# Kernel tuning notes

Hardware: AMD Instinct MI355X
Metric: run time of the kernel (lower is better)

## Reference

```python
import jax, jax.numpy as jnp
import numpy as np

D_MODEL = 512
NUM_HEADS = 8
D_K = D_MODEL // NUM_HEADS
D_FF = 2048
VOCAB = 32000
PAD_IDX = 0
SEQ = 2048
BATCH = 8
N_REPEAT = 6
# source computes ((d_model/num_heads)**1)/2 = 32.0 (precedence bug), not sqrt(d_k)
SCORE_DIV = (D_MODEL / NUM_HEADS) / 2.0
LN_EPS = 1e-5


def setup_inputs() -> dict:
    key = jax.random.key(0)
    ks = jax.random.split(key, 16)
    s = lambda fan_in: 1.0 / np.sqrt(fan_in)
    inp = {
        "ids": jax.random.randint(ks[0], (BATCH, SEQ), 0, VOCAB, dtype=jnp.int64)
               if jax.config.jax_enable_x64 else
               jax.random.randint(ks[0], (BATCH, SEQ), 0, VOCAB, dtype=jnp.int32),
        "emb": jax.random.normal(ks[1], (VOCAB, D_MODEL), jnp.float32),
        "Wq": jax.random.normal(ks[2], (D_MODEL, D_K), jnp.float32) * s(D_MODEL),
        "bq": jnp.zeros((D_K,), jnp.float32),
        "Wk": jax.random.normal(ks[3], (D_MODEL, D_K), jnp.float32) * s(D_MODEL),
        "bk": jnp.zeros((D_K,), jnp.float32),
        "Wv": jax.random.normal(ks[4], (D_MODEL, D_K), jnp.float32) * s(D_MODEL),
        "bv": jnp.zeros((D_K,), jnp.float32),
        "Wo": jax.random.normal(ks[5], (D_MODEL, D_MODEL), jnp.float32) * s(D_MODEL),
        "bo": jnp.zeros((D_MODEL,), jnp.float32),
        "W1": jax.random.normal(ks[6], (D_MODEL, D_FF), jnp.float32) * s(D_MODEL),
        "b1": jnp.zeros((D_FF,), jnp.float32),
        "W2": jax.random.normal(ks[7], (D_FF, D_MODEL), jnp.float32) * s(D_FF),
        "b2": jnp.zeros((D_MODEL,), jnp.float32),
    }
    # padding_idx row is zero in torch's nn.Embedding
    inp["emb"] = inp["emb"].at[PAD_IDX].set(0.0)
    return inp


def positional_encoding(seq_len, d_model):
    pos = jnp.arange(seq_len, dtype=jnp.float32)[:, None]          # [S,1]
    even_i = jnp.arange(0, d_model, 2, dtype=jnp.float32)          # actual indices 0,2,4,...
    odd_i = jnp.arange(1, d_model, 2, dtype=jnp.float32)
    pe_even = jnp.sin(pos / jnp.power(10000.0, 2.0 * even_i / d_model))  # [S,D/2]
    pe_odd = jnp.cos(pos / jnp.power(10000.0, 2.0 * odd_i / d_model))    # [S,D/2]
    pe = jnp.stack([pe_even, pe_odd], axis=2).reshape(seq_len, d_model)  # interleave
    return pe[None]  # [1,S,D]


def whole_tensor_layernorm(x):
    # F.layer_norm(x, normalized_shape=x.shape): normalize over ALL elems, no affine
    m = jnp.mean(x)
    v = jnp.mean(jnp.square(x - m))
    return (x - m) * jax.lax.rsqrt(v + LN_EPS)


def encoder_forward(ids, emb, Wq, bq, Wk, bk, Wv, bv, Wo, bo, W1, b1, W2, b2):
    mask = (ids != PAD_IDX)[..., None].astype(emb.dtype)
    x = emb[ids] * mask + positional_encoding(ids.shape[1], D_MODEL)  # [B,S,D]
    for _ in range(N_REPEAT):  # same weights reused every repeat (as in source)
        # all heads use the SAME q/k/v Linear -> compute once, tile NUM_HEADS times
        q = jnp.einsum("bsd,dk->bsk", x, Wq) + bq   # [B,S,64]
        k = jnp.einsum("bsd,dk->bsk", x, Wk) + bk
        v = jnp.einsum("bsd,dk->bsk", x, Wv) + bv
        scores = jnp.einsum("bsk,btk->bst", q, k) / SCORE_DIV  # [B,S,S]
        attn = jax.nn.softmax(scores, axis=-1)
        head = jnp.einsum("bst,btk->bsk", attn, v)             # [B,S,64]
        concat = jnp.tile(head, (1, 1, NUM_HEADS))             # [B,S,512]
        mha = jnp.einsum("bsd,de->bse", concat, Wo) + bo
        x1 = whole_tensor_layernorm(mha + x)
        ff = jnp.einsum("bsd,df->bsf", jax.nn.relu(jnp.einsum("bsd,df->bsf", x1, W1) + b1), W2) + b2
        x = whole_tensor_layernorm(x1 + ff)
    return x


def reference(ids, emb, Wq, bq, Wk, bk, Wv, bv, Wo, bo, W1, b1, W2, b2):
    return encoder_forward(ids, emb, Wq, bq, Wk, bk, Wv, bv, Wo, bo, W1, b1, W2, b2)
```

## Files before the change

kernel.cpp:

```cpp
#include <hip/hip_runtime.h>
#include <math.h>

#define BB 8
#define SS 2048
#define DM 512
#define DK 64
#define DFF 2048
#define ROWS (BB*SS)
#define NTOT (ROWS*DM)
#define LN_EPS 1e-5
#define PAD_IDX 0

typedef __attribute__((ext_vector_type(8))) short short8;
typedef __attribute__((ext_vector_type(4))) short s16x4;
typedef __attribute__((ext_vector_type(4))) float f32x4;

__device__ __forceinline__ short f2b(float f) {
    unsigned u = __float_as_uint(f);
    unsigned r = (u + 0x7fffu + ((u >> 16) & 1u)) >> 16;
    return (short)r;
}
__device__ __forceinline__ float b2f(short s) {
    return __uint_as_float(((unsigned)(unsigned short)s) << 16);
}

__global__ __launch_bounds__(256) void embed_kernel(const int* __restrict__ ids,
                                                    const float* __restrict__ emb,
                                                    short* __restrict__ T1,
                                                    double* __restrict__ red) {
    int idx = blockIdx.x * 256 + threadIdx.x;
    if (idx < 24) red[idx] = 0.0;
    if (idx >= NTOT) return;
    int d   = idx & (DM - 1);
    int row = idx >> 9;
    int s   = row & (SS - 1);
    int id  = ids[row];
    float e = (id != PAD_IDX) ? emb[(size_t)id * DM + d] : 0.0f;
    float ex  = 2.0f * (float)d / 512.0f;
    float div = powf(10000.0f, ex);
    float arg = (float)s / div;
    float pe  = (d & 1) ? cosf(arg) : sinf(arg);
    T1[idx] = f2b(e + pe);
}

__global__ __launch_bounds__(256) void packqkvT_kernel(const float* __restrict__ Wq,
                                                       const float* __restrict__ Wk,
                                                       const float* __restrict__ Wv,
                                                       const float* __restrict__ bq,
                                                       const float* __restrict__ bk,
                                                       const float* __restrict__ bv,
                                                       short* __restrict__ WqkvT,
                                                       float* __restrict__ bqkv) {
    int i = blockIdx.x * 256 + threadIdx.x;
    if (i < 256 * 512) {
        int n = i >> 9, k = i & 511;
        float v = (n < 64)  ? Wq[k * 64 + n]
                : (n < 128) ? Wk[k * 64 + (n - 64)]
                : (n < 192) ? Wv[k * 64 + (n - 128)] : 0.0f;
        WqkvT[i] = f2b(v);
    }
    if (i < 256)
        bqkv[i] = (i < 64) ? bq[i] : (i < 128) ? bk[i - 64] : (i < 192) ? bv[i - 128] : 0.0f;
}

__global__ __launch_bounds__(256) void wosumT_kernel(const float* __restrict__ Wo,
                                                     short* __restrict__ WoST) {
    int i = blockIdx.x * 256 + threadIdx.x;
    if (i >= 512 * 64) return;
    int e = i >> 6, k = i & 63;
    float s = 0.f;
#pragma unroll
    for (int h = 0; h < 8; ++h) s += Wo[(size_t)(h * 64 + k) * 512 + e];
    WoST[i] = f2b(s);
}

__global__ __launch_bounds__(256) void transpose_b16(const float* __restrict__ in,
                                                     short* __restrict__ out,
                                                     int R, int C) {
    __shared__ float tile[32][33];
    int bx = blockIdx.x * 32;
    int by = blockIdx.y * 32;
    int tx = threadIdx.x & 31, ty = threadIdx.x >> 5;
#pragma unroll
    for (int i = 0; i < 32; i += 8)
        tile[ty + i][tx] = in[(size_t)(by + ty + i) * C + bx + tx];
    __syncthreads();
#pragma unroll
    for (int i = 0; i < 32; i += 8)
        out[(size_t)(bx + ty + i) * R + by + tx] = f2b(tile[tx][ty + i]);
}

__global__ __launch_bounds__(256) void colsum_kernel(const short* __restrict__ WqkvT,
                                                     const short* __restrict__ W1T,
                                                     float* __restrict__ csq,
                                                     float* __restrict__ csw1) {
    int i = blockIdx.x * 256 + threadIdx.x;
    if (i < 256) {
        const short* p = WqkvT + (size_t)i * 512;
        float s = 0.f;
        for (int k = 0; k < 512; ++k) s += b2f(p[k]);
        csq[i] = s;
    } else if (i < 2304) {
        int n = i - 256;
        const short* p = W1T + (size_t)n * 512;
        float s = 0.f;
        for (int k = 0; k < 512; ++k) s += b2f(p[k]);
        csw1[n] = s;
    }
}

__global__ __launch_bounds__(256) void vtrans_kernel(const short* __restrict__ qkvb,
                                                     short* __restrict__ Vtg) {
    __shared__ short tile[32][40];
    int sx = blockIdx.x * 32;
    int dy = blockIdx.y * 32;
    int b  = blockIdx.z;
    int tx = threadIdx.x & 31, ty = threadIdx.x >> 5;
#pragma unroll
    for (int i = 0; i < 32; i += 8)
        tile[ty + i][tx] = qkvb[(size_t)(b * SS + sx + ty + i) * 256 + 128 + dy + tx];
    __syncthreads();
#pragma unroll
    for (int i = 0; i < 32; i += 8)
        Vtg[(size_t)(b * 64 + dy + ty + i) * SS + sx + tx] = tile[tx][ty + i];
}

__device__ __forceinline__ void async16(const void* g, void* l) {
    __builtin_amdgcn_global_load_lds(
        (const __attribute__((address_space(1))) void*)g,
        (__attribute__((address_space(3))) void*)l, 16, 0, 0);
}

template <bool RELU, bool RESID, bool STATS, bool FOLD, int BM, int BN, int BK>
__global__ __launch_bounds__(256) void gemm_mfma(const short* __restrict__ A,
                                                 const short* __restrict__ BT,
                                                 const float* __restrict__ bias,
                                                 const float* __restrict__ colsum,
                                                 const short* __restrict__ residB,
                                                 short* __restrict__ C,
                                                 const double* __restrict__ statsIn,
                                                 double* __restrict__ statsOut,
                                                 int M, int N, int K) {
    constexpr int NT   = (BN == 256) ? 4 : ((BM == 128) ? 4 : 2);
    constexpr int KSUB = BK / 32;
    constexpr int RPS  = (BK == 32) ? 64 : 32;
    constexpr int LPS  = (BM + BN) / RPS;
    __shared__ short As[2][BM * BK];
    __shared__ short Bs[2][BN * BK];
    const int t   = threadIdx.x;
    const int wv  = t >> 6;
    const int l   = t & 63;
    const int q   = l >> 4,  l16 = l & 15;
    const int mbase = (BM == 128) ? (wv >> 1) * 64 : 0;
    const int nbase = (BM == 128) ? (wv & 1) * 64
                    : ((BN == 256) ? wv * 64 : wv * 32);
    const long m0 = (long)blockIdx.x * BM;
    const long n0 = (long)blockIdx.y * BN;

    float muf = 0.f, rstdf = 1.f;
    if (FOLD || RESID) {
        if (statsIn) {
            double mean = statsIn[0] * (1.0 / NTOT);
            double var  = statsIn[1] * (1.0 / NTOT) - mean * mean;
            muf   = (float)mean;
            rstdf = (float)(1.0 / sqrt(var + LN_EPS));
        }
    }

    f32x4 acc[4][NT] = {};

    const int srow = (BK == 32) ? (wv * 16 + (l >> 2)) : (wv * 8 + (l >> 3));
    const int kcol = (BK == 32) ? (((l & 3) ^ ((l >> 3) & 3)) * 8)
                                : (((l & 7) ^ ((l >> 3) & 7)) * 8);
    const int wrow = (BK == 32) ? wv * 16 : wv * 8;

    auto stage = [&](int buf, int k0) {
#pragma unroll
        for (int i = 0; i < BM / RPS; ++i)
            async16(A + (m0 + srow + i * RPS) * (long)K + k0 + kcol,
                    &As[buf][(wrow + i * RPS) * BK + l * 8]);
#pragma unroll
        for (int i = 0; i < BN / RPS; ++i)
            async16(BT + (n0 + srow + i * RPS) * (long)K + k0 + kcol,
                    &Bs[buf][(wrow + i * RPS) * BK + l * 8]);
    };

    stage(0, 0);
    if (K > BK) stage(1, BK);
    int cur = 0;
    for (int k0 = 0; k0 < K; k0 += BK) {
        if (k0 + BK < K) {
            if constexpr (LPS == 3)       asm volatile("s_waitcnt vmcnt(3)" ::: "memory");
            else if constexpr (LPS == 4)  asm volatile("s_waitcnt vmcnt(4)" ::: "memory");
            else if constexpr (LPS == 6)  asm volatile("s_waitcnt vmcnt(6)" ::: "memory");
            else if constexpr (LPS == 8)  asm volatile("s_waitcnt vmcnt(8)" ::: "memory");
            else                          asm volatile("s_waitcnt vmcnt(10)" ::: "memory");
        } else {
            asm volatile("s_waitcnt vmcnt(0)" ::: "memory");
        }
        __builtin_amdgcn_sched_barrier(0);
        __builtin_amdgcn_s_barrier();
        __builtin_amdgcn_sched_barrier(0);

        short8 af[KSUB][4], bfr[KSUB][NT];
#pragma unroll
        for (int ks = 0; ks < KSUB; ++ks) {
            const int slot = (BK == 32) ? (q ^ ((l16 >> 1) & 3))
                                        : ((ks * 4 + q) ^ (l16 & 7));
#pragma unroll
            for (int i = 0; i < 4; ++i)
                af[ks][i] = *(const short8*)&As[cur][(mbase + i * 16 + l16) * BK + slot * 8];
#pragma unroll
            for (int i = 0; i < NT; ++i)
                bfr[ks][i] = *(const short8*)&Bs[cur][(nbase + i * 16 + l16) * BK + slot * 8];
        }
        asm volatile("s_waitcnt lgkmcnt(0)" ::: "memory");
        __builtin_amdgcn_sched_barrier(0);
        __builtin_amdgcn_s_barrier();
        __builtin_amdgcn_sched_barrier(0);

        if (k0 + 2 * BK < K) stage(cur, k0 + 2 * BK);

        __builtin_amdgcn_s_setprio(1);
#pragma unroll
        for (int ks = 0; ks < KSUB; ++ks)
#pragma unroll
            for (int mt = 0; mt < 4; ++mt)
#pragma unroll
                for (int nt = 0; nt < NT; ++nt)
                    acc[mt][nt] = __builtin_amdgcn_mfma_f32_16x16x32_bf16(
                        af[ks][mt], bfr[ks][nt], acc[mt][nt], 0, 0, 0);
        __builtin_amdgcn_s_setprio(0);
        cur ^= 1;
    }

    const float mr = muf * rstdf;
    float s = 0.f, sq = 0.f;
#pragma unroll
    for (int mt = 0; mt < 4; ++mt) {
        const long rowb = m0 + mbase + mt * 16 + q * 4;
#pragma unroll
        for (int nt = 0; nt < NT; ++nt) {
            const long col = n0 + nbase + nt * 16 + l16;
            const float bv = bias[col];
            const float cs = FOLD ? colsum[col] : 0.f;
#pragma unroll
            for (int r = 0; r < 4; ++r) {
                const long idx = (rowb + r) * (long)N + col;
                float v = acc[mt][nt][r];
                if (FOLD) v = rstdf * v + bv - mr * cs;
                else      v = v + bv;
                if (RESID) v += (b2f(residB[idx]) - muf) * rstdf;
                if (RELU)  v = fmaxf(v, 0.0f);
                if (STATS) { s += v; sq += v * v; }
                C[idx] = f2b(v);
            }
        }
    }
    if (STATS) {
#pragma unroll
        for (int o = 32; o; o >>= 1) {
            s  += __shfl_down(s, o);
            sq += __shfl_down(sq, o);
        }
        float* sm = (float*)As;
        if (l == 0) { sm[wv] = s; sm[4 + wv] = sq; }
        __syncthreads();
        if (t == 0) {
            atomicAdd(&statsOut[0], (double)(sm[0] + sm[1] + sm[2] + sm[3]));
            atomicAdd(&statsOut[1], (double)(sm[4] + sm[5] + sm[6] + sm[7]));
        }
    }
}

__global__ __launch_bounds__(256) void attn_mfma(const short* __restrict__ qkvb,
                                                 const short* __restrict__ Vtg,
                                                 short* __restrict__ head) {
    const int b  = blockIdx.y;
    const int q0 = blockIdx.x * 64;
    const int t  = threadIdx.x;
    const int w  = t >> 6;
    const int l  = t & 63;
    const int l15 = l & 15, lq = l >> 4;
    const int l7  = l & 7,  l8 = l >> 3;

    __shared__ short Ks[64][72];
    __shared__ short Vs[64][72];
    __shared__ short Ps[4][16][68];

    short8 qf[2];
    {
        const short* qrow = qkvb + (size_t)(b * SS + q0 + w * 16 + l15) * 256;
        qf[0] = *(const short8*)(qrow + lq * 8);
        qf[1] = *(const short8*)(qrow + 32 + lq * 8);
    }

    f32x4 acc[4];
#pragma unroll
    for (int mt = 0; mt < 4; ++mt) acc[mt] = {0.f, 0.f, 0.f, 0.f};
    float m_i = -INFINITY, l_i = 0.f;
    const float sc = 0.0450712500463f;

    short8 kreg[2], vreg[2];
    {
        const short* kb = qkvb + (size_t)(b * SS) * 256 + 64;
        kreg[0] = *(const short8*)(kb + (size_t)(w * 8 + l8) * 256 + l7 * 8);
        kreg[1] = *(const short8*)(kb + (size_t)(32 + w * 8 + l8) * 256 + l7 * 8);
        const short* vb = Vtg + (size_t)b * 64 * SS;
        vreg[0] = *(const short8*)(vb + (size_t)(w * 8 + l8) * SS + l7 * 8);
        vreg[1] = *(const short8*)(vb + (size_t)(32 + w * 8 + l8) * SS + l7 * 8);
    }

    for (int kt = 0; kt < SS / 64; ++kt) {
        __syncthreads();
        *(short8*)&Ks[w * 8 + l8][l7 * 8]      = kreg[0];
        *(short8*)&Ks[32 + w * 8 + l8][l7 * 8] = kreg[1];
        *(short8*)&Vs[w * 8 + l8][l7 * 8]      = vreg[0];
        *(short8*)&Vs[32 + w * 8 + l8][l7 * 8] = vreg[1];
        if (kt + 1 < SS / 64) {
            const short* kb = qkvb + (size_t)(b * SS + (kt + 1) * 64) * 256 + 64;
            kreg[0] = *(const short8*)(kb + (size_t)(w * 8 + l8) * 256 + l7 * 8);
            kreg[1] = *(const short8*)(kb + (size_t)(32 + w * 8 + l8) * 256 + l7 * 8);
            const short* vb = Vtg + (size_t)b * 64 * SS + (kt + 1) * 64;
            vreg[0] = *(const short8*)(vb + (size_t)(w * 8 + l8) * SS + l7 * 8);
            vreg[1] = *(const short8*)(vb + (size_t)(32 + w * 8 + l8) * SS + l7 * 8);
        }
        __syncthreads();

        f32x4 st[4];
#pragma unroll
        for (int mt = 0; mt < 4; ++mt) st[mt] = {0.f, 0.f, 0.f, 0.f};
#pragma unroll
        for (int kc = 0; kc < 2; ++kc)
#pragma unroll
            for (int mt = 0; mt < 4; ++mt) {
                short8 kf = *(const short8*)&Ks[mt * 16 + l15][kc * 32 + lq * 8];
                st[mt] = __builtin_amdgcn_mfma_f32_16x16x32_bf16(kf, qf[kc], st[mt], 0, 0, 0);
            }
        float mx = m_i;
#pragma unroll
        for (int mt = 0; mt < 4; ++mt)
#pragma unroll
            for (int r = 0; r < 4; ++r) {
                st[mt][r] *= sc;
                mx = fmaxf(mx, st[mt][r]);
            }
        mx = fmaxf(mx, __shfl_xor(mx, 16));
        mx = fmaxf(mx, __shfl_xor(mx, 32));
        float alpha = exp2f(m_i - mx);
        float rs = 0.f;
#pragma unroll
        for (int mt = 0; mt < 4; ++mt) {
            s16x4 pk;
#pragma unroll
            for (int r = 0; r < 4; ++r) {
                float p = exp2f(st[mt][r] - mx);
                rs += p;
                pk[r] = f2b(p);
            }
            *(s16x4*)&Ps[w][l15][mt * 16 + lq * 4] = pk;
        }
        rs += __shfl_xor(rs, 16);
        rs += __shfl_xor(rs, 32);
        l_i = l_i * alpha + rs;
        m_i = mx;
#pragma unroll
        for (int mt = 0; mt < 4; ++mt)
#pragma unroll
            for (int r = 0; r < 4; ++r) acc[mt][r] *= alpha;

#pragma unroll
        for (int kc = 0; kc < 2; ++kc) {
            s16x4 p0 = *(const s16x4*)&Ps[w][l15][kc * 32 + lq * 8];
            s16x4 p1 = *(const s16x4*)&Ps[w][l15][kc * 32 + lq * 8 + 4];
            short8 pf = __builtin_shufflevector(p0, p1, 0, 1, 2, 3, 4, 5, 6, 7);
#pragma unroll
            for (int mt = 0; mt < 4; ++mt) {
                short8 vf = *(const short8*)&Vs[mt * 16 + l15][kc * 32 + lq * 8];
                acc[mt] = __builtin_amdgcn_mfma_f32_16x16x32_bf16(vf, pf, acc[mt], 0, 0, 0);
            }
        }
    }
    float inv = 1.0f / l_i;
    short* out = head + (size_t)(b * SS + q0 + w * 16 + l15) * 64;
#pragma unroll
    for (int mt = 0; mt < 4; ++mt) {
        s16x4 o;
#pragma unroll
        for (int r = 0; r < 4; ++r) o[r] = f2b(acc[mt][r] * inv);
        *(s16x4*)&out[mt * 16 + lq * 4] = o;
    }
}

__global__ __launch_bounds__(256) void lnfinal_kernel(const short* __restrict__ y,
                                                      float* __restrict__ out,
                                                      const double* __restrict__ red,
                                                      int n) {
    double mean = red[0] / n;
    double var  = red[1] / n - mean * mean;
    float mu   = (float)mean;
    float rstd = (float)(1.0 / sqrt(var + LN_EPS));
    for (int i = blockIdx.x * blockDim.x + threadIdx.x; i < n;
         i += gridDim.x * blockDim.x)
        out[i] = (b2f(y[i]) - mu) * rstd;
}

extern "C" void kernel_launch(void* const* d_in, const int* in_sizes, int n_in,
                              void* d_out, int out_size, void* d_ws, size_t ws_size,
                              hipStream_t stream) {
    const int*   ids = (const int*)d_in[0];
    const float* emb = (const float*)d_in[1];
    const float* Wq  = (const float*)d_in[2];
    const float* bq  = (const float*)d_in[3];
    const float* Wk  = (const float*)d_in[4];
    const float* bk  = (const float*)d_in[5];
    const float* Wv  = (const float*)d_in[6];
    const float* bv  = (const float*)d_in[7];
    const float* Wo  = (const float*)d_in[8];
    const float* bo  = (const float*)d_in[9];
    const float* W1  = (const float*)d_in[10];
    const float* b1  = (const float*)d_in[11];
    const float* W2  = (const float*)d_in[12];
    const float* b2  = (const float*)d_in[13];

    float* xout = (float*)d_out;
    char* w = (char*)d_ws;

    const bool big = ws_size >= (size_t)105195712 + 256;

    short *qkvb, *Vtg, *head, *T1, *T2, *hch, *WqkvT, *WoST, *W1T, *W2T;
    float *bqkv, *csq, *csw1; double* red;

    if (big) {
        hch   = (short*)(w + 0);
        qkvb  = (short*)(w + 0);
        Vtg   = (short*)(w + 8388608);
        head  = (short*)(w + 10485760);
        T1    = (short*)(w + 67108864);
        T2    = (short*)(w + 83886080);
        WqkvT = (short*)(w + 100663296);
        bqkv  = (float*)(w + 100925440);
        csq   = (float*)(w + 100926464);
        WoST  = (short*)(w + 100927488);
        W1T   = (short*)(w + 100993024);
        csw1  = (float*)(w + 103090176);
        W2T   = (short*)(w + 103098368);
        red   = (double*)(w + 105195520);
    } else {
        hch   = (short*)(w + 0);
        qkvb  = (short*)(w + 0);
        Vtg   = (short*)(w + 8388608);
        head  = (short*)(w + 10485760);
        T1    = (short*)(w + 33554432);
        T2    = (short*)(w + 50331648);
        WqkvT = (short*)(w + 67108864);
        bqkv  = (float*)(w + 67371008);
        csq   = (float*)(w + 67372032);
        WoST  = (short*)(w + 67373056);
        W1T   = (short*)(w + 67438592);
        csw1  = (float*)(w + 69535744);
        W2T   = (short*)(w + 69543936);
        red   = (double*)(w + 71641088);
    }

    packqkvT_kernel<<<(256 * 512 + 255) / 256, 256, 0, stream>>>(Wq, Wk, Wv, bq, bk, bv, WqkvT, bqkv);
    wosumT_kernel<<<(512 * 64 + 255) / 256, 256, 0, stream>>>(Wo, WoST);
    transpose_b16<<<dim3(2048 / 32, 512 / 32), 256, 0, stream>>>(W1, W1T, 512, 2048);
    transpose_b16<<<dim3(512 / 32, 2048 / 32), 256, 0, stream>>>(W2, W2T, 2048, 512);
    colsum_kernel<<<9, 256, 0, stream>>>(WqkvT, W1T, csq, csw1);
    embed_kernel<<<NTOT / 256, 256, 0, stream>>>(ids, emb, T1, red);

    for (int rep = 0; rep < 6; ++rep) {
        const double* sprev = rep ? red + 4 * (rep - 1) + 2 : nullptr;
        double* red1 = red + 4 * rep;
        double* red2 = red + 4 * rep + 2;

        gemm_mfma<false, false, false, true, 64, 128, 64><<<dim3(256, 2), 256, 0, stream>>>(
            T1, WqkvT, bqkv, csq, nullptr, qkvb, sprev, nullptr, ROWS, 256, DM);
        vtrans_kernel<<<dim3(SS / 32, 2, BB), 256, 0, stream>>>(qkvb, Vtg);
        attn_mfma<<<dim3(SS / 64, BB), 256, 0, stream>>>(qkvb, Vtg, head);
        gemm_mfma<false, true, true, false, 64, 128, 64><<<dim3(256, 4), 256, 0, stream>>>(
            head, WoST, bo, nullptr, T1, T2, sprev, red1, ROWS, DM, DK);
        if (big) {
            gemm_mfma<true, false, false, true, 128, 128, 64><<<dim3(128, 16), 256, 0, stream>>>(
                T2, W1T, b1, csw1, nullptr, hch, red1, nullptr, ROWS, DFF, DM);
            gemm_mfma<false, true, true, false, 64, 256, 64><<<dim3(256, 2), 256, 0, stream>>>(
                hch, W2T, b2, nullptr, T2, T1, red1, red2, ROWS, DM, DFF);
        } else {
            for (int c = 0; c < 2; ++c) {
                const size_t off = (size_t)c * 8192 * DM;
                gemm_mfma<true, false, false, true, 128, 128, 64><<<dim3(64, 16), 256, 0, stream>>>(
                    T2 + off, W1T, b1, csw1, nullptr, hch, red1, nullptr, 8192, DFF, DM);
                gemm_mfma<false, true, true, false, 64, 256, 64><<<dim3(128, 2), 256, 0, stream>>>(
                    hch, W2T, b2, nullptr, T2 + off, T1 + off, red1, red2, 8192, DM, DFF);
            }
        }
    }
    lnfinal_kernel<<<4096, 256, 0, stream>>>(T1, xout, red + 4 * 5 + 2, NTOT);
}
```

Before: 1.200 ms.

## Add LDS-free direct-load MFMA GEMM for QKV, output-projection and FFN2 GEMMs

Adds a gemm_direct kernel in which each wave loads its bf16 A and B fragments straight from global memory into registers and issues MFMA without LDS staging or barriers. The QKV projection, the Wo projection and the second FFN GEMM now use it with new tile shapes, keeping the fused LayerNorm fold, residual and stats epilogues. The aim is to cut LDS traffic and synchronisation overhead. In exchange there is no data reuse across waves, so A fragments are loaded redundantly by each wave and global/L2 traffic rises, especially for the K=2048 FFN2 GEMM.

```diff
diff --git a/kernel.cpp b/kernel.cpp
--- a/kernel.cpp
+++ b/kernel.cpp
@@ -123,6 +123,103 @@
 #pragma unroll
     for (int i = 0; i < 32; i += 8)
         Vtg[(size_t)(b * 64 + dy + ty + i) * SS + sx + tx] = tile[tx][ty + i];
+}
+
+template <bool RELU, bool RESID, bool STATS, bool FOLD, int BM, int BN, int K>
+__global__ __launch_bounds__(256) void gemm_direct(const short* __restrict__ A,
+                                                   const short* __restrict__ BT,
+                                                   const float* __restrict__ bias,
+                                                   const float* __restrict__ colsum,
+                                                   const short* __restrict__ residB,
+                                                   short* __restrict__ C,
+                                                   const double* __restrict__ statsIn,
+                                                   double* __restrict__ statsOut,
+                                                   int M, int N) {
+    constexpr int MT = BM / 16;
+    constexpr int NW = BN / 4;
+    constexpr int NT = NW / 16;
+    __shared__ float sm[8];
+    const int t  = threadIdx.x;
+    const int wv = t >> 6;
+    const int l  = t & 63;
+    const int q  = l >> 4, l16 = l & 15;
+    const int nbase = wv * NW;
+    const long m0 = (long)blockIdx.x * BM;
+    const long n0 = (long)blockIdx.y * BN;
+
+    float muf = 0.f, rstdf = 1.f;
+    if (FOLD || RESID) {
+        if (statsIn) {
+            double mean = statsIn[0] * (1.0 / NTOT);
+            double var  = statsIn[1] * (1.0 / NTOT) - mean * mean;
+            muf   = (float)mean;
+            rstdf = (float)(1.0 / sqrt(var + LN_EPS));
+        }
+    }
+
+    f32x4 acc[MT][NT] = {};
+
+    const short* pA = A  + (m0 + l16) * (long)K + q * 8;
+    const short* pB = BT + (n0 + nbase + l16) * (long)K + q * 8;
+
+    for (int k0 = 0; k0 < K; k0 += 64) {
+        short8 af[2][MT], bfr[2][NT];
+#pragma unroll
+        for (int ks = 0; ks < 2; ++ks)
+#pragma unroll
+            for (int i = 0; i < MT; ++i)
+                af[ks][i] = *(const short8*)(pA + (long)i * 16 * K + k0 + ks * 32);
+#pragma unroll
+        for (int ks = 0; ks < 2; ++ks)
+#pragma unroll
+            for (int i = 0; i < NT; ++i)
+                bfr[ks][i] = *(const short8*)(pB + (long)i * 16 * K + k0 + ks * 32);
+#pragma unroll
+        for (int ks = 0; ks < 2; ++ks)
+#pragma unroll
+            for (int mt = 0; mt < MT; ++mt)
+#pragma unroll
+                for (int nt = 0; nt < NT; ++nt)
+                    acc[mt][nt] = __builtin_amdgcn_mfma_f32_16x16x32_bf16(
+                        af[ks][mt], bfr[ks][nt], acc[mt][nt], 0, 0, 0);
+    }
+
+    const float mr = muf * rstdf;
+    float s = 0.f, sq = 0.f;
+#pragma unroll
+    for (int mt = 0; mt < MT; ++mt) {
+        const long rowb = m0 + mt * 16 + q * 4;
+#pragma unroll
+        for (int nt = 0; nt < NT; ++nt) {
+            const long col = n0 + nbase + nt * 16 + l16;
+            const float bv = bias[col];
+            const float cs = FOLD ? colsum[col] : 0.f;
+#pragma unroll
+            for (int r = 0; r < 4; ++r) {
+                const long idx = (rowb + r) * (long)N + col;
+                float v = acc[mt][nt][r];
+                if (FOLD) v = rstdf * v + bv - mr * cs;
+                else      v = v + bv;
+                if (RESID) v += (b2f(residB[idx]) - muf) * rstdf;
+                if (RELU)  v = fmaxf(v, 0.0f);
+                if (STATS) { s += v; sq += v * v; }
+                C[idx] = f2b(v);
+            }
+        }
+    }
+    if (STATS) {
+#pragma unroll
+        for (int o = 32; o; o >>= 1) {
+            s  += __shfl_down(s, o);
+            sq += __shfl_down(sq, o);
+        }
+        if (l == 0) { sm[wv] = s; sm[4 + wv] = sq; }
+        __syncthreads();
+        if (t == 0) {
+            atomicAdd(&statsOut[0], (double)(sm[0] + sm[1] + sm[2] + sm[3]));
+            atomicAdd(&statsOut[1], (double)(sm[4] + sm[5] + sm[6] + sm[7]));
+        }
+    }
 }
 
 __device__ __forceinline__ void async16(const void* g, void* l) {
@@ -475,24 +572,24 @@
         double* red1 = red + 4 * rep;
         double* red2 = red + 4 * rep + 2;
 
-        gemm_mfma<false, false, false, true, 64, 128, 64><<<dim3(256, 2), 256, 0, stream>>>(
-            T1, WqkvT, bqkv, csq, nullptr, qkvb, sprev, nullptr, ROWS, 256, DM);
+        gemm_direct<false, false, false, true, 64, 64, 512><<<dim3(256, 4), 256, 0, stream>>>(
+            T1, WqkvT, bqkv, csq, nullptr, qkvb, sprev, nullptr, ROWS, 256);
         vtrans_kernel<<<dim3(SS / 32, 2, BB), 256, 0, stream>>>(qkvb, Vtg);
         attn_mfma<<<dim3(SS / 64, BB), 256, 0, stream>>>(qkvb, Vtg, head);
-        gemm_mfma<false, true, true, false, 64, 128, 64><<<dim3(256, 4), 256, 0, stream>>>(
-            head, WoST, bo, nullptr, T1, T2, sprev, red1, ROWS, DM, DK);
+        gemm_direct<false, true, true, false, 64, 128, 64><<<dim3(256, 4), 256, 0, stream>>>(
+            head, WoST, bo, nullptr, T1, T2, sprev, red1, ROWS, DM);
         if (big) {
             gemm_mfma<true, false, false, true, 128, 128, 64><<<dim3(128, 16), 256, 0, stream>>>(
                 T2, W1T, b1, csw1, nullptr, hch, red1, nullptr, ROWS, DFF, DM);
-            gemm_mfma<false, true, true, false, 64, 256, 64><<<dim3(256, 2), 256, 0, stream>>>(
-                hch, W2T, b2, nullptr, T2, T1, red1, red2, ROWS, DM, DFF);
+            gemm_direct<false, true, true, false, 64, 128, 2048><<<dim3(256, 4), 256, 0, stream>>>(
+                hch, W2T, b2, nullptr, T2, T1, red1, red2, ROWS, DM);
         } else {
             for (int c = 0; c < 2; ++c) {
                 const size_t off = (size_t)c * 8192 * DM;
                 gemm_mfma<true, false, false, true, 128, 128, 64><<<dim3(64, 16), 256, 0, stream>>>(
                     T2 + off, W1T, b1, csw1, nullptr, hch, red1, nullptr, 8192, DFF, DM);
-                gemm_mfma<false, true, true, false, 64, 256, 64><<<dim3(128, 2), 256, 0, stream>>>(
-                    hch, W2T, b2, nullptr, T2 + off, T1 + off, red1, red2, 8192, DM, DFF);
+                gemm_direct<false, true, true, false, 64, 128, 2048><<<dim3(128, 4), 256, 0, stream>>>(
+                    hch, W2T, b2, nullptr, T2 + off, T1 + off, red1, red2, 8192, DM);
             }
         }
     }
```

Result: slower. 2.542 ms (+111.8%).
